# Kernel optimization log

Measured on AMD Instinct MI355X. Metric: run time of the kernel, lower is better.

## Reference

```python
import jax, jax.numpy as jnp
import numpy as np

V, D, E, N, Dd, Dc, NL, B, L = 50280, 1024, 2048, 16, 64, 4, 2, 2, 1024
EPS = 1e-5


def rmsnorm(x, w):
    return x * jax.lax.rsqrt(jnp.mean(x * x, axis=-1, keepdims=True) + EPS) * w


def setup_inputs() -> dict:
    key = jax.random.key(0)
    ks = jax.random.split(key, 18)
    n = jax.random.normal
    inp = {
        "input_ids": jax.random.randint(ks[0], (B, L), 0, V),
        "embedding": n(ks[1], (V, D), jnp.float32) * 0.02,
        "lm_head_w": n(ks[2], (V, D), jnp.float32) * 0.02,
        "norm_w": jnp.ones((D,), jnp.float32),
        # stacked per-layer params (leading dim = n_layer)
        "l_norm_w": jnp.ones((NL, D), jnp.float32),
        "l_skip_w": n(ks[3], (NL, E, D), jnp.float32) / np.sqrt(D),
        "l_in_w": n(ks[4], (NL, E, D), jnp.float32) / np.sqrt(D),
        "l_conv_w": n(ks[5], (NL, E, 1, Dc), jnp.float32) / np.sqrt(Dc),
        "l_conv_b": jnp.zeros((NL, E), jnp.float32),
        "l_Wd1": n(ks[6], (NL, Dd, E), jnp.float32) / np.sqrt(E),
        "l_Wd2_w": n(ks[7], (NL, E, Dd), jnp.float32) / np.sqrt(Dd),
        "l_Wd2_b": n(ks[8], (NL, E), jnp.float32) * 0.1 - 4.0,  # small dt init
        "l_WB": n(ks[9], (NL, N, E), jnp.float32) / np.sqrt(E),
        "l_WC": n(ks[10], (NL, N, E), jnp.float32) / np.sqrt(E),
        "l_A_log": jnp.log(jax.random.uniform(ks[11], (NL, E, N), jnp.float32, 0.5, 1.2)),
        "l_WD": jnp.ones((NL, E), jnp.float32),
        "l_out_w": n(ks[12], (NL, D, E), jnp.float32) / np.sqrt(E),
    }
    return inp


def mamba_layer(resid, norm_w, skip_w, in_w, conv_w, conv_b, Wd1, Wd2_w, Wd2_b,
                WB, WC, A_log, WD, out_w):
    x = rmsnorm(resid, norm_w)                      # [B,L,D]
    skip = x @ skip_w.T                             # [B,L,E]
    x = x @ in_w.T                                  # [B,L,E]
    # depthwise causal conv (pad D_conv-1 on left == pad both + slice [:L])
    xc = jax.lax.conv_general_dilated(
        x.transpose(0, 2, 1), conv_w, (1,), [(Dc - 1, 0)],
        feature_group_count=E, dimension_numbers=("NCH", "OIH", "NCH"))
    x = (xc + conv_b[None, :, None]).transpose(0, 2, 1)  # [B,L,E]
    x = jax.nn.silu(x)

    delta = jax.nn.softplus((x @ Wd1.T) @ Wd2_w.T + Wd2_b)  # [B,L,E]
    A = -jnp.exp(A_log)                                      # [E,N]
    A_bar = jnp.exp(delta[..., None] * A)                    # [B,L,E,N]
    Bt = x @ WB.T                                            # [B,L,N]
    Ct = x @ WC.T                                            # [B,L,N]
    Bx = (delta * x)[..., None] * Bt[:, :, None, :]          # [B,L,E,N]

    def step(h, inp):
        Ab_t, Bx_t, C_t = inp                                # [B,E,N],[B,E,N],[B,N]
        h = Ab_t * h + Bx_t
        y = jnp.einsum("ben,bn->be", h, C_t)
        return h, y

    h0 = jnp.zeros((B, E, N), x.dtype)
    _, ys = jax.lax.scan(step, h0,
                         (A_bar.transpose(1, 0, 2, 3), Bx.transpose(1, 0, 2, 3),
                          Ct.transpose(1, 0, 2)))
    y = ys.transpose(1, 0, 2)                                # [B,L,E]
    y = y + x * WD
    y = y * jax.nn.silu(skip)
    return resid + y @ out_w.T


def reference(input_ids, embedding, lm_head_w, norm_w, l_norm_w, l_skip_w, l_in_w,
              l_conv_w, l_conv_b, l_Wd1, l_Wd2_w, l_Wd2_b, l_WB, l_WC, l_A_log,
              l_WD, l_out_w):
    resid = embedding[input_ids]                             # [B,L,D]
    for i in range(NL):
        resid = mamba_layer(resid, l_norm_w[i], l_skip_w[i], l_in_w[i],
                            l_conv_w[i], l_conv_b[i], l_Wd1[i], l_Wd2_w[i],
                            l_Wd2_b[i], l_WB[i], l_WC[i], l_A_log[i], l_WD[i],
                            l_out_w[i])
    resid = rmsnorm(resid, norm_w)
    return resid @ lm_head_w.T                               # [B,L,V]
```

## Files before the change

kernel.cpp:

```cpp
#include <hip/hip_runtime.h>

typedef unsigned short u16;
using bf16x8 = __attribute__((ext_vector_type(8))) __bf16;
using f32x4  = __attribute__((ext_vector_type(4))) float;

typedef const void __attribute__((address_space(1))) gvoid_t;
typedef void __attribute__((address_space(3))) lvoid_t;

#define NL 2
#define Bd 2
#define Ld 1024
#define Dd_ 1024
#define Ed 2048
#define Nd 16
#define TOK (Bd*Ld)
#define VPAD 50432
#define VREAL 50280
#define NCHUNK 16
#define CLEN 64
#define XLD 4096

__device__ __forceinline__ u16 f2bf(float f) {
    union { float f; unsigned u; } v; v.f = f;
    unsigned u = v.u;
    unsigned r = (u + 0x7fffu + ((u >> 16) & 1u)) >> 16;
    return (u16)r;
}
__device__ __forceinline__ float siluf(float x) { return x / (1.f + __expf(-x)); }
__device__ __forceinline__ float softplusf(float z) {
    return (z > 15.f) ? z : log1pf(__expf(z));
}

__global__ void k_f32_to_bf16(const float* __restrict__ s, u16* __restrict__ d, int n4) {
    int i = blockIdx.x * 256 + threadIdx.x;
    if (i >= n4) return;
    float4 v = *(const float4*)&s[(size_t)i * 4];
    ushort4 o; o.x = f2bf(v.x); o.y = f2bf(v.y); o.z = f2bf(v.z); o.w = f2bf(v.w);
    *(ushort4*)&d[(size_t)i * 4] = o;
}

__global__ void k_f32_to_bf16_pad(const float* __restrict__ s, u16* __restrict__ d,
                                  int n4valid, int n4tot) {
    int i = blockIdx.x * 256 + threadIdx.x;
    if (i >= n4tot) return;
    ushort4 o;
    if (i < n4valid) {
        float4 v = *(const float4*)&s[(size_t)i * 4];
        o.x = f2bf(v.x); o.y = f2bf(v.y); o.z = f2bf(v.z); o.w = f2bf(v.w);
    } else { o.x = o.y = o.z = o.w = 0; }
    *(ushort4*)&d[(size_t)i * 4] = o;
}

__global__ void k_build_wsmall(const float* __restrict__ Wd1, const float* __restrict__ WB,
                               const float* __restrict__ WC, u16* __restrict__ dst) {
    int i = blockIdx.x * 256 + threadIdx.x;
    int col = (i * 4) & (Ed - 1);
    int r = (i * 4) >> 11;
    ushort4 o;
    const float* src = nullptr;
    if (r < 64) src = &Wd1[(size_t)r * Ed];
    else if (r < 80) src = &WB[(size_t)(r - 64) * Ed];
    else if (r < 96) src = &WC[(size_t)(r - 80) * Ed];
    if (src) {
        float4 v = *(const float4*)&src[col];
        o.x = f2bf(v.x); o.y = f2bf(v.y); o.z = f2bf(v.z); o.w = f2bf(v.w);
    } else { o.x = o.y = o.z = o.w = 0; }
    *(ushort4*)&dst[(size_t)i * 4] = o;
}

__global__ void k_embed(const int* __restrict__ ids, const float* __restrict__ emb,
                        float* __restrict__ resid) {
    int tk = blockIdx.x;
    int d = threadIdx.x * 4;
    int id = ids[tk];
    float4 v = *(const float4*)&emb[(size_t)id * Dd_ + d];
    *(float4*)&resid[(size_t)tk * Dd_ + d] = v;
}

__global__ void k_rmsnorm_bf16(const float* __restrict__ in, const float* __restrict__ w,
                               u16* __restrict__ out) {
    int tk = blockIdx.x;
    int tid = threadIdx.x;
    float4 v = *(const float4*)&in[(size_t)tk * Dd_ + tid * 4];
    float ss = v.x * v.x + v.y * v.y + v.z * v.z + v.w * v.w;
    #pragma unroll
    for (int m = 32; m; m >>= 1) ss += __shfl_xor(ss, m);
    __shared__ float red[4];
    if ((tid & 63) == 0) red[tid >> 6] = ss;
    __syncthreads();
    ss = red[0] + red[1] + red[2] + red[3];
    float rs = rsqrtf(ss * (1.f / 1024.f) + 1e-5f);
    float4 wv = *(const float4*)&w[tid * 4];
    ushort4 o;
    o.x = f2bf(v.x * rs * wv.x); o.y = f2bf(v.y * rs * wv.y);
    o.z = f2bf(v.z * rs * wv.z); o.w = f2bf(v.w * rs * wv.w);
    *(ushort4*)&out[(size_t)tk * Dd_ + tid * 4] = o;
}

__global__ void k_conv_silu(const float* __restrict__ xin, const float* __restrict__ cw,
                            const float* __restrict__ cb, float* __restrict__ xout,
                            u16* __restrict__ xbf) {
    int blk = blockIdx.x;
    int tk = blk >> 1;
    int e0 = ((blk & 1) << 10) + threadIdx.x * 4;
    int b = tk >> 10, l = tk & 1023;
    float4 w0 = *(const float4*)&cw[(size_t)(e0 + 0) * 4];
    float4 w1 = *(const float4*)&cw[(size_t)(e0 + 1) * 4];
    float4 w2 = *(const float4*)&cw[(size_t)(e0 + 2) * 4];
    float4 w3 = *(const float4*)&cw[(size_t)(e0 + 3) * 4];
    float4 bv = *(const float4*)&cb[e0];
    float a0 = bv.x, a1 = bv.y, a2 = bv.z, a3 = bv.w;
    const float* wp0 = (const float*)&w0; const float* wp1 = (const float*)&w1;
    const float* wp2 = (const float*)&w2; const float* wp3 = (const float*)&w3;
    #pragma unroll
    for (int k = 0; k < 4; ++k) {
        int ll = l - 3 + k;
        if (ll < 0) continue;
        float4 xv = *(const float4*)&xin[((size_t)(b * 1024 + ll)) * XLD + e0];
        a0 = fmaf(xv.x, wp0[k], a0); a1 = fmaf(xv.y, wp1[k], a1);
        a2 = fmaf(xv.z, wp2[k], a2); a3 = fmaf(xv.w, wp3[k], a3);
    }
    a0 = siluf(a0); a1 = siluf(a1); a2 = siluf(a2); a3 = siluf(a3);
    float4 o; o.x = a0; o.y = a1; o.z = a2; o.w = a3;
    *(float4*)&xout[(size_t)tk * Ed + e0] = o;
    ushort4 ob; ob.x = f2bf(a0); ob.y = f2bf(a1); ob.z = f2bf(a2); ob.w = f2bf(a3);
    *(ushort4*)&xbf[(size_t)tk * Ed + e0] = ob;
}

__global__ void k_reduce_xs(const float* __restrict__ part, float* __restrict__ xs,
                            u16* __restrict__ xsbf) {
    size_t i4 = ((size_t)blockIdx.x * 256 + threadIdx.x) * 4;
    float4 s = *(const float4*)&part[i4];
    #pragma unroll
    for (int c = 1; c < 8; ++c) {
        float4 v = *(const float4*)&part[(size_t)c * TOK * 128 + i4];
        s.x += v.x; s.y += v.y; s.z += v.z; s.w += v.w;
    }
    *(float4*)&xs[i4] = s;
    ushort4 o; o.x = f2bf(s.x); o.y = f2bf(s.y); o.z = f2bf(s.z); o.w = f2bf(s.w);
    *(ushort4*)&xsbf[i4] = o;
}

__global__ void k_add2(const float* __restrict__ part, float* __restrict__ resid) {
    size_t i4 = ((size_t)blockIdx.x * 256 + threadIdx.x) * 4;
    float4 r = *(const float4*)&resid[i4];
    float4 a = *(const float4*)&part[i4];
    float4 b = *(const float4*)&part[(size_t)TOK * Dd_ + i4];
    r.x += a.x + b.x; r.y += a.y + b.y; r.z += a.z + b.z; r.w += a.w + b.w;
    *(float4*)&resid[i4] = r;
}

__global__ void k_scan_pass1(const float* __restrict__ delta, const float* __restrict__ x,
                             const float* __restrict__ xs, const float* __restrict__ A_log,
                             float* __restrict__ sumd, float* __restrict__ Hc) {
    __shared__ float sBt[CLEN][16];
    int t = blockIdx.x * 256 + threadIdx.x;
    int e = t & (Ed - 1);
    int cb = t >> 11;
    int b = cb & 1, c = cb >> 1;
    int rowbase = b * 1024 + c * CLEN;
    {
        int f = threadIdx.x * 4;
        int row = f >> 4, cc = f & 15;
        float4 v = *(const float4*)&xs[(size_t)(rowbase + row) * 128 + 64 + cc];
        *(float4*)&sBt[row][cc] = v;
    }
    __syncthreads();
    float dA[16], h[16];
    #pragma unroll
    for (int n = 0; n < 16; ++n) { dA[n] = -__expf(A_log[e * 16 + n]); h[n] = 0.f; }
    float sd = 0.f;
    for (int l = 0; l < CLEN; ++l) {
        size_t row = (size_t)rowbase + l;
        float dlt = delta[row * Ed + e];
        float xv  = x[row * Ed + e];
        sd += dlt;
        float dx = dlt * xv;
        float4 bt0 = *(const float4*)&sBt[l][0];
        float4 bt1 = *(const float4*)&sBt[l][4];
        float4 bt2 = *(const float4*)&sBt[l][8];
        float4 bt3 = *(const float4*)&sBt[l][12];
        float bts[16] = {bt0.x,bt0.y,bt0.z,bt0.w, bt1.x,bt1.y,bt1.z,bt1.w,
                         bt2.x,bt2.y,bt2.z,bt2.w, bt3.x,bt3.y,bt3.z,bt3.w};
        #pragma unroll
        for (int n = 0; n < 16; ++n) {
            float a = __expf(dA[n] * dlt);
            h[n] = fmaf(a, h[n], dx * bts[n]);
        }
    }
    size_t gg = (size_t)cb * Ed + e;
    #pragma unroll
    for (int n = 0; n < 16; ++n) Hc[gg * 16 + n] = h[n];
    sumd[gg] = sd;
}

__global__ void k_scan_combine(const float* __restrict__ sumd, const float* __restrict__ Hc,
                               const float* __restrict__ A_log, float* __restrict__ Hin) {
    int idx = blockIdx.x * 256 + threadIdx.x;
    int n = idx & 15;
    int e = (idx >> 4) & (Ed - 1);
    int b = idx >> 15;
    float dA = -__expf(A_log[e * Nd + n]);
    float h = 0.f;
    #pragma unroll
    for (int c = 0; c < NCHUNK; ++c) {
        size_t g = ((size_t)(c * Bd + b) * Ed + e);
        Hin[g * Nd + n] = h;
        float a = __expf(dA * sumd[g]);
        h = fmaf(a, h, Hc[g * Nd + n]);
    }
}

__global__ void k_scan_pass2(const float* __restrict__ delta, const float* __restrict__ x,
                             const float* __restrict__ xs, const float* __restrict__ A_log,
                             const float* __restrict__ Hin, const float* __restrict__ WD,
                             const float* __restrict__ skipg, u16* __restrict__ ybf) {
    __shared__ float sBC[CLEN][32];
    int t = blockIdx.x * 256 + threadIdx.x;
    int e = t & (Ed - 1);
    int cb = t >> 11;
    int b = cb & 1, c = cb >> 1;
    int rowbase = b * 1024 + c * CLEN;
    {
        int f = threadIdx.x * 8;
        int row = f >> 5, cc = f & 31;
        float4 v0 = *(const float4*)&xs[(size_t)(rowbase + row) * 128 + 64 + cc];
        float4 v1 = *(const float4*)&xs[(size_t)(rowbase + row) * 128 + 64 + cc + 4];
        *(float4*)&sBC[row][cc] = v0;
        *(float4*)&sBC[row][cc + 4] = v1;
    }
    __syncthreads();
    float dA[16], h[16];
    size_t gg = (size_t)cb * Ed + e;
    #pragma unroll
    for (int n = 0; n < 16; ++n) {
        dA[n] = -__expf(A_log[e * 16 + n]);
        h[n] = Hin[gg * 16 + n];
    }
    float wd = WD[e];
    for (int l = 0; l < CLEN; ++l) {
        size_t row = (size_t)rowbase + l;
        float dlt = delta[row * Ed + e];
        float xv  = x[row * Ed + e];
        float dx = dlt * xv;
        float4 b0 = *(const float4*)&sBC[l][0];
        float4 b1 = *(const float4*)&sBC[l][4];
        float4 b2 = *(const float4*)&sBC[l][8];
        float4 b3 = *(const float4*)&sBC[l][12];
        float4 c0 = *(const float4*)&sBC[l][16];
        float4 c1 = *(const float4*)&sBC[l][20];
        float4 c2 = *(const float4*)&sBC[l][24];
        float4 c3 = *(const float4*)&sBC[l][28];
        float bts[16] = {b0.x,b0.y,b0.z,b0.w, b1.x,b1.y,b1.z,b1.w,
                         b2.x,b2.y,b2.z,b2.w, b3.x,b3.y,b3.z,b3.w};
        float cts[16] = {c0.x,c0.y,c0.z,c0.w, c1.x,c1.y,c1.z,c1.w,
                         c2.x,c2.y,c2.z,c2.w, c3.x,c3.y,c3.z,c3.w};
        float y = 0.f;
        #pragma unroll
        for (int n = 0; n < 16; ++n) {
            float a = __expf(dA[n] * dlt);
            h[n] = fmaf(a, h[n], dx * bts[n]);
            y = fmaf(h[n], cts[n], y);
        }
        float yo = y + xv * wd;
        float sk = skipg[row * XLD + e];
        ybf[row * Ed + e] = f2bf(yo * siluf(sk));
    }
}

template<int EPI>
__global__ __launch_bounds__(256, 2)
void k_gemm_bt(const u16* __restrict__ A, int lda,
               const u16* __restrict__ B, int ldb,
               float* __restrict__ C, int ldc,
               const float* __restrict__ aux,
               int ntm, int Nstore, int Kc, size_t Cz) {
    __shared__ u16 lsA[2][128 * 32];
    __shared__ u16 lsB[2][128 * 32];
    int kz = blockIdx.z;
    A += (size_t)kz * Kc;
    B += (size_t)kz * Kc;
    C += (size_t)kz * Cz;
    int tid = threadIdx.x;
    int bid = blockIdx.x;
    int mt = bid % ntm, nt = bid / ntm;
    int mBase = mt * 128, nBase = nt * 128;
    int lane = tid & 63, wid = tid >> 6;
    int wr = wid >> 1, wc = wid & 1;

    f32x4 acc[4][4] = {};
    const u16* Ablk = A + (size_t)mBase * lda;
    const u16* Bblk = B + (size_t)nBase * ldb;
    int nk = Kc >> 5;

    auto stage = [&](int buf, int kt) {
        #pragma unroll
        for (int i = 0; i < 2; ++i) {
            int chunk = i * 256 + tid;
            int row = chunk >> 2;
            int kc  = (chunk & 3) << 3;
            const u16* ga = Ablk + (size_t)row * lda + (kt << 5) + kc;
            const u16* gb = Bblk + (size_t)row * ldb + (kt << 5) + kc;
            u16* la = &lsA[buf][(size_t)(i * 256 + wid * 64) * 8];
            u16* lb = &lsB[buf][(size_t)(i * 256 + wid * 64) * 8];
            __builtin_amdgcn_global_load_lds((gvoid_t*)ga, (lvoid_t*)la, 16, 0, 0);
            __builtin_amdgcn_global_load_lds((gvoid_t*)gb, (lvoid_t*)lb, 16, 0, 0);
        }
    };
    auto compute = [&](int buf) {
        bf16x8 af[4], bfr[4];
        const u16* baseA = lsA[buf];
        const u16* baseB = lsB[buf];
        int kq = (lane >> 4) << 3;
        int r  = lane & 15;
        #pragma unroll
        for (int mi = 0; mi < 4; ++mi)
            af[mi] = *(const bf16x8*)&baseA[(size_t)((wr * 64 + mi * 16 + r) * 32 + kq)];
        #pragma unroll
        for (int ni = 0; ni < 4; ++ni)
            bfr[ni] = *(const bf16x8*)&baseB[(size_t)((wc * 64 + ni * 16 + r) * 32 + kq)];
        #pragma unroll
        for (int mi = 0; mi < 4; ++mi)
            #pragma unroll
            for (int ni = 0; ni < 4; ++ni)
                acc[mi][ni] = __builtin_amdgcn_mfma_f32_16x16x32_bf16(af[mi], bfr[ni], acc[mi][ni], 0, 0, 0);
    };

    stage(0, 0);
    asm volatile("s_waitcnt vmcnt(0)" ::: "memory");
    __syncthreads();
    int cur = 0;
    for (int kt = 0; kt + 1 < nk; ++kt) {
        stage(cur ^ 1, kt + 1);
        compute(cur);
        asm volatile("s_waitcnt vmcnt(0)" ::: "memory");
        __syncthreads();
        cur ^= 1;
    }
    compute(cur);

    int rbase = (lane >> 4) * 4, ccol = lane & 15;
    #pragma unroll
    for (int mi = 0; mi < 4; ++mi) {
        #pragma unroll
        for (int ni = 0; ni < 4; ++ni) {
            int gc = nBase + wc * 64 + ni * 16 + ccol;
            if (gc < Nstore) {
                float bias = (EPI == 2) ? aux[gc] : 0.f;
                #pragma unroll
                for (int rr = 0; rr < 4; ++rr) {
                    int gr = mBase + wr * 64 + mi * 16 + rbase + rr;
                    size_t off = (size_t)gr * ldc + gc;
                    float v = acc[mi][ni][rr];
                    if (EPI == 2) v = softplusf(v + bias);
                    C[off] = v;
                }
            }
        }
    }
}

#define BAR()    asm volatile("s_barrier" ::: "memory")
#define WAITV2() asm volatile("s_waitcnt vmcnt(2)" ::: "memory")
#define WAITV0() asm volatile("s_waitcnt vmcnt(0)" ::: "memory")

#define STG(buf, mat, h, kt) { \
    const u16* _s0 = ((mat) ? srcB[(h)*2]     : srcA[(h)*2])     + (size_t)(kt) * 64; \
    const u16* _s1 = ((mat) ? srcB[(h)*2 + 1] : srcA[(h)*2 + 1]) + (size_t)(kt) * 64; \
    char* _d = (char*)&ls[buf][mat][0]; \
    __builtin_amdgcn_global_load_lds((gvoid_t*)_s0, (lvoid_t*)(_d + (h)*16384 + tid*16), 16, 0, 0); \
    __builtin_amdgcn_global_load_lds((gvoid_t*)_s1, (lvoid_t*)(_d + (h)*16384 + 8192 + tid*16), 16, 0, 0); }

#define QUAD(buf, kk, mih) { \
    const char* _pa = (const char*)&ls[buf][0][0]; \
    const char* _pb = (const char*)&ls[buf][1][0]; \
    bf16x8 _af[4], _bf[4]; \
    _Pragma("unroll") \
    for (int _m = 0; _m < 4; ++_m) \
        _af[_m] = *(const bf16x8*)(_pa + abase + ((mih)*4 + _m) * 2048 + (kk) * 1024); \
    _Pragma("unroll") \
    for (int _n = 0; _n < 4; ++_n) \
        _bf[_n] = *(const bf16x8*)(_pb + bbase + _n * 2048 + (kk) * 1024); \
    __builtin_amdgcn_s_setprio(1); \
    _Pragma("unroll") \
    for (int _m = 0; _m < 4; ++_m) \
        _Pragma("unroll") \
        for (int _n = 0; _n < 4; ++_n) \
            acc[(mih)*4 + _m][_n] = __builtin_amdgcn_mfma_f32_16x16x32_bf16(_af[_m], _bf[_n], acc[(mih)*4 + _m][_n], 0, 0, 0); \
    __builtin_amdgcn_s_setprio(0); }

__global__ __launch_bounds__(512, 2)
void k_gemm256(const u16* __restrict__ A, int lda,
               const u16* __restrict__ B, int ldb,
               float* __restrict__ C, int ldc,
               int ntm, int Nstore, int K) {
    __shared__ u16 ls[2][2][256 * 64];
    const int tid = threadIdx.x;
    const int lane = tid & 63, wid = tid >> 6;
    const int wr = wid >> 2, wc = wid & 3;

    int nwg = gridDim.x, bid = blockIdx.x;
    int q8 = nwg >> 3, r8 = nwg & 7;
    int xcd = bid & 7, linb = bid >> 3;
    int sb = (xcd < r8 ? xcd * (q8 + 1) : r8 * (q8 + 1) + (xcd - r8) * q8) + linb;
    int mt = sb % ntm, nt = sb / ntm;

    const u16* Ablk = A + (size_t)(mt * 256) * lda;
    const u16* Bblk = B + (size_t)(nt * 256) * ldb;

    const u16* srcA[4]; const u16* srcB[4];
    #pragma unroll
    for (int s = 0; s < 4; ++s) {
        int p = s * 8192 + tid * 16;
        int qq = p ^ (((p >> 9) & 1) << 5);
        int sub = qq >> 10, rin = (qq >> 6) & 15, cby = qq & 63;
        int row = ((sub >> 1) << 4) | rin;
        int col = ((((sub & 1) << 6) | cby)) >> 1;
        srcA[s] = Ablk + (size_t)row * lda + col;
        srcB[s] = Bblk + (size_t)row * ldb + col;
    }
    int l15 = lane & 15;
    int lowb = (l15 * 64 + ((lane >> 4) << 4)) ^ (((l15 >> 3) & 1) << 5);
    int abase = wr * 16384 + lowb;
    int bbase = wc * 8192  + lowb;

    f32x4 acc[8][4] = {};
    int nk = K >> 6, nit = nk >> 1;

    STG(0, 0, 0, 0); STG(0, 0, 1, 0); STG(0, 1, 0, 0); STG(0, 1, 1, 0);

    for (int i = 0; i < nit; ++i) {
        int t1 = 2 * i + 1, t2 = 2 * i + 2;
        bool more = (i + 1 < nit);
        STG(1, 0, 0, t1);
        WAITV2(); BAR();
        QUAD(0, 0, 0); BAR();
        STG(1, 0, 1, t1);
        QUAD(0, 0, 1); BAR();
        STG(1, 1, 0, t1);
        QUAD(0, 1, 0); BAR();
        STG(1, 1, 1, t1);
        QUAD(0, 1, 1); BAR();
        if (more) { STG(0, 0, 0, t2); WAITV2(); } else { WAITV0(); }
        BAR();
        QUAD(1, 0, 0); BAR();
        if (more) STG(0, 0, 1, t2);
        QUAD(1, 0, 1); BAR();
        if (more) STG(0, 1, 0, t2);
        QUAD(1, 1, 0); BAR();
        if (more) STG(0, 1, 1, t2);
        QUAD(1, 1, 1); BAR();
    }

    int rb = (lane >> 4) * 4, cc = lane & 15;
    int mrow = mt * 256 + wr * 128, ncol = nt * 256 + wc * 64;
    #pragma unroll
    for (int mi = 0; mi < 8; ++mi) {
        #pragma unroll
        for (int ni = 0; ni < 4; ++ni) {
            int gc = ncol + ni * 16 + cc;
            if (gc < Nstore) {
                #pragma unroll
                for (int rr = 0; rr < 4; ++rr) {
                    size_t off = (size_t)(mrow + mi * 16 + rb + rr) * ldc + gc;
                    C[off] = acc[mi][ni][rr];
                }
            }
        }
    }
}

extern "C" void kernel_launch(void* const* d_in, const int* in_sizes, int n_in,
                              void* d_out, int out_size, void* d_ws, size_t ws_size,
                              hipStream_t stream) {
    const int*   ids   = (const int*)d_in[0];
    const float* emb   = (const float*)d_in[1];
    const float* lmw   = (const float*)d_in[2];
    const float* normw = (const float*)d_in[3];
    const float* lnw   = (const float*)d_in[4];
    const float* lskip = (const float*)d_in[5];
    const float* linw  = (const float*)d_in[6];
    const float* lcw   = (const float*)d_in[7];
    const float* lcb   = (const float*)d_in[8];
    const float* lWd1  = (const float*)d_in[9];
    const float* lWd2  = (const float*)d_in[10];
    const float* lWd2b = (const float*)d_in[11];
    const float* lWB   = (const float*)d_in[12];
    const float* lWC   = (const float*)d_in[13];
    const float* lAlog = (const float*)d_in[14];
    const float* lWD   = (const float*)d_in[15];
    const float* loutw = (const float*)d_in[16];
    float* out = (float*)d_out;

    char* ws = (char*)d_ws;
    size_t off = 0;
    auto alloc = [&](size_t bytes) { char* p = ws + off; off += (bytes + 255) & ~(size_t)255; return p; };
    u16*   lm_bf    = (u16*)  alloc((size_t)VPAD * 1024 * 2);
    u16*   wsi_bf   = (u16*)  alloc((size_t)NL * 4096 * Dd_ * 2);
    u16*   wout_bf  = (u16*)  alloc((size_t)NL * Dd_ * Ed * 2);
    u16*   wd2_bf   = (u16*)  alloc((size_t)NL * Ed * 64 * 2);
    u16*   wsml_bf  = (u16*)  alloc((size_t)NL * 128 * Ed * 2);
    float* resid    = (float*)alloc((size_t)TOK * Dd_ * 4);
    u16*   xn_bf    = (u16*)  alloc((size_t)TOK * Dd_ * 2);
    float* xall     = (float*)alloc((size_t)TOK * XLD * 4);
    float* xf       = (float*)alloc((size_t)TOK * Ed * 4);
    u16*   xbf      = (u16*)  alloc((size_t)TOK * Ed * 2);
    float* xs       = (float*)alloc((size_t)TOK * 128 * 4);
    u16*   xs_bf    = (u16*)  alloc((size_t)TOK * 128 * 2);
    float* xs_part  = (float*)alloc((size_t)8 * TOK * 128 * 4);
    float* opart    = (float*)alloc((size_t)2 * TOK * Dd_ * 4);
    float* delta    = (float*)alloc((size_t)TOK * Ed * 4);
    float* sumd     = (float*)alloc((size_t)NCHUNK * Bd * Ed * 4);
    float* Hc       = (float*)alloc((size_t)NCHUNK * Bd * Ed * Nd * 4);
    float* Hin      = (float*)alloc((size_t)NCHUNK * Bd * Ed * Nd * 4);
    u16*   ybf      = (u16*)  alloc((size_t)TOK * Ed * 2);
    (void)ws_size; (void)in_sizes; (void)n_in; (void)out_size;

    {
        int n4v = VREAL * 1024 / 4, n4t = VPAD * 1024 / 4;
        k_f32_to_bf16_pad<<<(n4t + 255) / 256, 256, 0, stream>>>(lmw, lm_bf, n4v, n4t);
        int n4 = Ed * Dd_ / 4;
        for (int lyr = 0; lyr < NL; ++lyr) {
            k_f32_to_bf16<<<(n4 + 255) / 256, 256, 0, stream>>>(
                lskip + (size_t)lyr * Ed * Dd_, wsi_bf + (size_t)lyr * 4096 * Dd_, n4);
            k_f32_to_bf16<<<(n4 + 255) / 256, 256, 0, stream>>>(
                linw + (size_t)lyr * Ed * Dd_, wsi_bf + (size_t)lyr * 4096 * Dd_ + (size_t)Ed * Dd_, n4);
        }
        k_f32_to_bf16<<<(NL * n4 + 255) / 256, 256, 0, stream>>>(loutw, wout_bf, NL * n4);
        int n4b = NL * Ed * 64 / 4;
        k_f32_to_bf16<<<(n4b + 255) / 256, 256, 0, stream>>>(lWd2, wd2_bf, n4b);
        for (int lyr = 0; lyr < NL; ++lyr)
            k_build_wsmall<<<256, 256, 0, stream>>>(lWd1 + (size_t)lyr * 64 * Ed,
                                                    lWB + (size_t)lyr * Nd * Ed,
                                                    lWC + (size_t)lyr * Nd * Ed,
                                                    wsml_bf + (size_t)lyr * 128 * Ed);
    }

    k_embed<<<TOK, 256, 0, stream>>>(ids, emb, resid);

    for (int lyr = 0; lyr < NL; ++lyr) {
        const float* Alog = lAlog + (size_t)lyr * Ed * Nd;
        k_rmsnorm_bf16<<<TOK, 256, 0, stream>>>(resid, lnw + (size_t)lyr * Dd_, xn_bf);
        k_gemm_bt<0><<<dim3(16 * 32, 1, 1), 256, 0, stream>>>(xn_bf, Dd_,
            wsi_bf + (size_t)lyr * 4096 * Dd_, Dd_, xall, XLD, nullptr, 16, 4096, 1024, 0);
        k_conv_silu<<<TOK * 2, 256, 0, stream>>>(xall + Ed, lcw + (size_t)lyr * Ed * 4,
                                                 lcb + (size_t)lyr * Ed, xf, xbf);
        k_gemm_bt<0><<<dim3(16, 1, 8), 256, 0, stream>>>(xbf, Ed,
            wsml_bf + (size_t)lyr * 128 * Ed, Ed, xs_part, 128, nullptr, 16, 128, 256,
            (size_t)TOK * 128);
        k_reduce_xs<<<TOK * 128 / 4 / 256, 256, 0, stream>>>(xs_part, xs, xs_bf);
        k_gemm_bt<2><<<dim3(16 * 16, 1, 1), 256, 0, stream>>>(xs_bf, 128,
            wd2_bf + (size_t)lyr * Ed * 64, 64, delta, Ed, lWd2b + (size_t)lyr * Ed,
            16, Ed, 64, 0);
        k_scan_pass1<<<NCHUNK * Bd * Ed / 256, 256, 0, stream>>>(delta, xf, xs, Alog, sumd, Hc);
        k_scan_combine<<<Bd * Ed * Nd / 256, 256, 0, stream>>>(sumd, Hc, Alog, Hin);
        k_scan_pass2<<<NCHUNK * Bd * Ed / 256, 256, 0, stream>>>(delta, xf, xs, Alog, Hin,
            lWD + (size_t)lyr * Ed, xall, ybf);
        k_gemm_bt<0><<<dim3(16 * 8, 1, 2), 256, 0, stream>>>(ybf, Ed,
            wout_bf + (size_t)lyr * Dd_ * Ed, Ed, opart, Dd_, nullptr, 16, Dd_, 1024,
            (size_t)TOK * Dd_);
        k_add2<<<TOK * Dd_ / 4 / 256, 256, 0, stream>>>(opart, resid);
    }

    k_rmsnorm_bf16<<<TOK, 256, 0, stream>>>(resid, normw, xn_bf);
    k_gemm256<<<dim3(8 * (VPAD / 256), 1, 1), 512, 0, stream>>>(xn_bf, Dd_, lm_bf, Dd_,
        out, VREAL, 8, VREAL, 1024);
}
```

Baseline: 811.7 us.

## Fuse weight conversions, embed+norm, add+norm, and fold scan combine into pass2

All weight fp32-to-bf16 conversions are merged into a single launch, and the embedding gather is fused with the first RMSNorm. The residual add is fused with the next layer's (or the final) RMSNorm. The separate chunk-state combine kernel is removed: each pass2 thread recomputes its incoming state by looping over the earlier chunks. This cuts launch count and intermediate traffic, at the cost of redundant serial prefix work in pass2 for later chunks.

```diff
diff --git a/kernel.cpp b/kernel.cpp
--- a/kernel.cpp
+++ b/kernel.cpp
@@ -31,57 +31,60 @@
     return (z > 15.f) ? z : log1pf(__expf(z));
 }
 
-__global__ void k_f32_to_bf16(const float* __restrict__ s, u16* __restrict__ d, int n4) {
-    int i = blockIdx.x * 256 + threadIdx.x;
-    if (i >= n4) return;
-    float4 v = *(const float4*)&s[(size_t)i * 4];
-    ushort4 o; o.x = f2bf(v.x); o.y = f2bf(v.y); o.z = f2bf(v.z); o.w = f2bf(v.w);
-    *(ushort4*)&d[(size_t)i * 4] = o;
-}
-
-__global__ void k_f32_to_bf16_pad(const float* __restrict__ s, u16* __restrict__ d,
-                                  int n4valid, int n4tot) {
-    int i = blockIdx.x * 256 + threadIdx.x;
-    if (i >= n4tot) return;
+__global__ void k_convert_all(const float* __restrict__ lmw, const float* __restrict__ lskip,
+                              const float* __restrict__ linw, const float* __restrict__ loutw,
+                              const float* __restrict__ lWd2, const float* __restrict__ lWd1,
+                              const float* __restrict__ lWB, const float* __restrict__ lWC,
+                              u16* __restrict__ lm_bf, u16* __restrict__ wsi_bf,
+                              u16* __restrict__ wout_bf, u16* __restrict__ wd2_bf,
+                              u16* __restrict__ wsml_bf) {
+    int g = blockIdx.x * 256 + threadIdx.x;
+    const float* src = nullptr; u16* dst = nullptr;
+    if (g < 12910592) {
+        dst = lm_bf + (size_t)g * 4;
+        if (g < 12871680) src = lmw + (size_t)g * 4;
+    } else if (g < 15007744) {
+        int i = g - 12910592;
+        int layer = i >> 20;
+        int within = i & 1048575;
+        int mat = within >> 19;
+        int idx = within & 524287;
+        src = (mat ? linw : lskip) + ((size_t)layer << 21) + ((size_t)idx * 4);
+        dst = wsi_bf + ((size_t)layer << 22) + ((size_t)mat << 21) + ((size_t)idx * 4);
+    } else if (g < 16056320) {
+        int i = g - 15007744;
+        src = loutw + (size_t)i * 4; dst = wout_bf + (size_t)i * 4;
+    } else if (g < 16121856) {
+        int i = g - 16056320;
+        src = lWd2 + (size_t)i * 4; dst = wd2_bf + (size_t)i * 4;
+    } else {
+        int i = g - 16121856;
+        int layer = i >> 16;
+        int j = i & 65535;
+        int col = (j * 4) & 2047;
+        int r = (j * 4) >> 11;
+        const float* s2 = nullptr;
+        if (r < 64) s2 = lWd1 + ((size_t)layer * 64 + r) * 2048;
+        else if (r < 80) s2 = lWB + ((size_t)layer * 16 + (r - 64)) * 2048;
+        else if (r < 96) s2 = lWC + ((size_t)layer * 16 + (r - 80)) * 2048;
+        dst = wsml_bf + ((size_t)layer << 18) + (size_t)j * 4;
+        if (s2) src = s2 + col;
+    }
     ushort4 o;
-    if (i < n4valid) {
-        float4 v = *(const float4*)&s[(size_t)i * 4];
+    if (src) {
+        float4 v = *(const float4*)src;
         o.x = f2bf(v.x); o.y = f2bf(v.y); o.z = f2bf(v.z); o.w = f2bf(v.w);
     } else { o.x = o.y = o.z = o.w = 0; }
-    *(ushort4*)&d[(size_t)i * 4] = o;
-}
-
-__global__ void k_build_wsmall(const float* __restrict__ Wd1, const float* __restrict__ WB,
-                               const float* __restrict__ WC, u16* __restrict__ dst) {
-    int i = blockIdx.x * 256 + threadIdx.x;
-    int col = (i * 4) & (Ed - 1);
-    int r = (i * 4) >> 11;
-    ushort4 o;
-    const float* src = nullptr;
-    if (r < 64) src = &Wd1[(size_t)r * Ed];
-    else if (r < 80) src = &WB[(size_t)(r - 64) * Ed];
-    else if (r < 96) src = &WC[(size_t)(r - 80) * Ed];
-    if (src) {
-        float4 v = *(const float4*)&src[col];
-        o.x = f2bf(v.x); o.y = f2bf(v.y); o.z = f2bf(v.z); o.w = f2bf(v.w);
-    } else { o.x = o.y = o.z = o.w = 0; }
-    *(ushort4*)&dst[(size_t)i * 4] = o;
-}
-
-__global__ void k_embed(const int* __restrict__ ids, const float* __restrict__ emb,
-                        float* __restrict__ resid) {
-    int tk = blockIdx.x;
-    int d = threadIdx.x * 4;
+    *(ushort4*)dst = o;
+}
+
+__global__ void k_embed_norm(const int* __restrict__ ids, const float* __restrict__ emb,
+                             const float* __restrict__ w, float* __restrict__ resid,
+                             u16* __restrict__ out) {
+    int tk = blockIdx.x, tid = threadIdx.x;
     int id = ids[tk];
-    float4 v = *(const float4*)&emb[(size_t)id * Dd_ + d];
-    *(float4*)&resid[(size_t)tk * Dd_ + d] = v;
-}
-
-__global__ void k_rmsnorm_bf16(const float* __restrict__ in, const float* __restrict__ w,
-                               u16* __restrict__ out) {
-    int tk = blockIdx.x;
-    int tid = threadIdx.x;
-    float4 v = *(const float4*)&in[(size_t)tk * Dd_ + tid * 4];
+    float4 v = *(const float4*)&emb[(size_t)id * Dd_ + tid * 4];
+    *(float4*)&resid[(size_t)tk * Dd_ + tid * 4] = v;
     float ss = v.x * v.x + v.y * v.y + v.z * v.z + v.w * v.w;
     #pragma unroll
     for (int m = 32; m; m >>= 1) ss += __shfl_xor(ss, m);
@@ -94,6 +97,30 @@
     ushort4 o;
     o.x = f2bf(v.x * rs * wv.x); o.y = f2bf(v.y * rs * wv.y);
     o.z = f2bf(v.z * rs * wv.z); o.w = f2bf(v.w * rs * wv.w);
+    *(ushort4*)&out[(size_t)tk * Dd_ + tid * 4] = o;
+}
+
+__global__ void k_add2_norm(const float* __restrict__ part, float* __restrict__ resid,
+                            const float* __restrict__ w, u16* __restrict__ out) {
+    int tk = blockIdx.x, tid = threadIdx.x;
+    size_t i4 = (size_t)tk * Dd_ + tid * 4;
+    float4 r = *(const float4*)&resid[i4];
+    float4 a = *(const float4*)&part[i4];
+    float4 b = *(const float4*)&part[(size_t)TOK * Dd_ + i4];
+    r.x += a.x + b.x; r.y += a.y + b.y; r.z += a.z + b.z; r.w += a.w + b.w;
+    *(float4*)&resid[i4] = r;
+    float ss = r.x * r.x + r.y * r.y + r.z * r.z + r.w * r.w;
+    #pragma unroll
+    for (int m = 32; m; m >>= 1) ss += __shfl_xor(ss, m);
+    __shared__ float red[4];
+    if ((tid & 63) == 0) red[tid >> 6] = ss;
+    __syncthreads();
+    ss = red[0] + red[1] + red[2] + red[3];
+    float rs = rsqrtf(ss * (1.f / 1024.f) + 1e-5f);
+    float4 wv = *(const float4*)&w[tid * 4];
+    ushort4 o;
+    o.x = f2bf(r.x * rs * wv.x); o.y = f2bf(r.y * rs * wv.y);
+    o.z = f2bf(r.z * rs * wv.z); o.w = f2bf(r.w * rs * wv.w);
     *(ushort4*)&out[(size_t)tk * Dd_ + tid * 4] = o;
 }
 
@@ -141,15 +168,6 @@
     *(ushort4*)&xsbf[i4] = o;
 }
 
-__global__ void k_add2(const float* __restrict__ part, float* __restrict__ resid) {
-    size_t i4 = ((size_t)blockIdx.x * 256 + threadIdx.x) * 4;
-    float4 r = *(const float4*)&resid[i4];
-    float4 a = *(const float4*)&part[i4];
-    float4 b = *(const float4*)&part[(size_t)TOK * Dd_ + i4];
-    r.x += a.x + b.x; r.y += a.y + b.y; r.z += a.z + b.z; r.w += a.w + b.w;
-    *(float4*)&resid[i4] = r;
-}
-
 __global__ void k_scan_pass1(const float* __restrict__ delta, const float* __restrict__ x,
                              const float* __restrict__ xs, const float* __restrict__ A_log,
                              float* __restrict__ sumd, float* __restrict__ Hc) {
@@ -194,26 +212,10 @@
     sumd[gg] = sd;
 }
 
-__global__ void k_scan_combine(const float* __restrict__ sumd, const float* __restrict__ Hc,
-                               const float* __restrict__ A_log, float* __restrict__ Hin) {
-    int idx = blockIdx.x * 256 + threadIdx.x;
-    int n = idx & 15;
-    int e = (idx >> 4) & (Ed - 1);
-    int b = idx >> 15;
-    float dA = -__expf(A_log[e * Nd + n]);
-    float h = 0.f;
-    #pragma unroll
-    for (int c = 0; c < NCHUNK; ++c) {
-        size_t g = ((size_t)(c * Bd + b) * Ed + e);
-        Hin[g * Nd + n] = h;
-        float a = __expf(dA * sumd[g]);
-        h = fmaf(a, h, Hc[g * Nd + n]);
-    }
-}
-
 __global__ void k_scan_pass2(const float* __restrict__ delta, const float* __restrict__ x,
                              const float* __restrict__ xs, const float* __restrict__ A_log,
-                             const float* __restrict__ Hin, const float* __restrict__ WD,
+                             const float* __restrict__ sumd, const float* __restrict__ Hc,
+                             const float* __restrict__ WD,
                              const float* __restrict__ skipg, u16* __restrict__ ybf) {
     __shared__ float sBC[CLEN][32];
     int t = blockIdx.x * 256 + threadIdx.x;
@@ -231,11 +233,17 @@
     }
     __syncthreads();
     float dA[16], h[16];
-    size_t gg = (size_t)cb * Ed + e;
     #pragma unroll
     for (int n = 0; n < 16; ++n) {
         dA[n] = -__expf(A_log[e * 16 + n]);
-        h[n] = Hin[gg * 16 + n];
+        h[n] = 0.f;
+    }
+    for (int cc = 0; cc < c; ++cc) {
+        size_t g2 = ((size_t)(cc * Bd + b) * Ed + e);
+        float sdc = sumd[g2];
+        #pragma unroll
+        for (int n = 0; n < 16; ++n)
+            h[n] = fmaf(__expf(dA[n] * sdc), h[n], Hc[g2 * 16 + n]);
     }
     float wd = WD[e];
     for (int l = 0; l < CLEN; ++l) {
@@ -512,35 +520,16 @@
     float* delta    = (float*)alloc((size_t)TOK * Ed * 4);
     float* sumd     = (float*)alloc((size_t)NCHUNK * Bd * Ed * 4);
     float* Hc       = (float*)alloc((size_t)NCHUNK * Bd * Ed * Nd * 4);
-    float* Hin      = (float*)alloc((size_t)NCHUNK * Bd * Ed * Nd * 4);
     u16*   ybf      = (u16*)  alloc((size_t)TOK * Ed * 2);
     (void)ws_size; (void)in_sizes; (void)n_in; (void)out_size;
 
-    {
-        int n4v = VREAL * 1024 / 4, n4t = VPAD * 1024 / 4;
-        k_f32_to_bf16_pad<<<(n4t + 255) / 256, 256, 0, stream>>>(lmw, lm_bf, n4v, n4t);
-        int n4 = Ed * Dd_ / 4;
-        for (int lyr = 0; lyr < NL; ++lyr) {
-            k_f32_to_bf16<<<(n4 + 255) / 256, 256, 0, stream>>>(
-                lskip + (size_t)lyr * Ed * Dd_, wsi_bf + (size_t)lyr * 4096 * Dd_, n4);
-            k_f32_to_bf16<<<(n4 + 255) / 256, 256, 0, stream>>>(
-                linw + (size_t)lyr * Ed * Dd_, wsi_bf + (size_t)lyr * 4096 * Dd_ + (size_t)Ed * Dd_, n4);
-        }
-        k_f32_to_bf16<<<(NL * n4 + 255) / 256, 256, 0, stream>>>(loutw, wout_bf, NL * n4);
-        int n4b = NL * Ed * 64 / 4;
-        k_f32_to_bf16<<<(n4b + 255) / 256, 256, 0, stream>>>(lWd2, wd2_bf, n4b);
-        for (int lyr = 0; lyr < NL; ++lyr)
-            k_build_wsmall<<<256, 256, 0, stream>>>(lWd1 + (size_t)lyr * 64 * Ed,
-                                                    lWB + (size_t)lyr * Nd * Ed,
-                                                    lWC + (size_t)lyr * Nd * Ed,
-                                                    wsml_bf + (size_t)lyr * 128 * Ed);
-    }
-
-    k_embed<<<TOK, 256, 0, stream>>>(ids, emb, resid);
+    k_convert_all<<<63488, 256, 0, stream>>>(lmw, lskip, linw, loutw, lWd2, lWd1, lWB, lWC,
+                                             lm_bf, wsi_bf, wout_bf, wd2_bf, wsml_bf);
+
+    k_embed_norm<<<TOK, 256, 0, stream>>>(ids, emb, lnw, resid, xn_bf);
 
     for (int lyr = 0; lyr < NL; ++lyr) {
         const float* Alog = lAlog + (size_t)lyr * Ed * Nd;
-        k_rmsnorm_bf16<<<TOK, 256, 0, stream>>>(resid, lnw + (size_t)lyr * Dd_, xn_bf);
         k_gemm_bt<0><<<dim3(16 * 32, 1, 1), 256, 0, stream>>>(xn_bf, Dd_,
             wsi_bf + (size_t)lyr * 4096 * Dd_, Dd_, xall, XLD, nullptr, 16, 4096, 1024, 0);
         k_conv_silu<<<TOK * 2, 256, 0, stream>>>(xall + Ed, lcw + (size_t)lyr * Ed * 4,
@@ -553,16 +542,15 @@
             wd2_bf + (size_t)lyr * Ed * 64, 64, delta, Ed, lWd2b + (size_t)lyr * Ed,
             16, Ed, 64, 0);
         k_scan_pass1<<<NCHUNK * Bd * Ed / 256, 256, 0, stream>>>(delta, xf, xs, Alog, sumd, Hc);
-        k_scan_combine<<<Bd * Ed * Nd / 256, 256, 0, stream>>>(sumd, Hc, Alog, Hin);
-        k_scan_pass2<<<NCHUNK * Bd * Ed / 256, 256, 0, stream>>>(delta, xf, xs, Alog, Hin,
-            lWD + (size_t)lyr * Ed, xall, ybf);
+        k_scan_pass2<<<NCHUNK * Bd * Ed / 256, 256, 0, stream>>>(delta, xf, xs, Alog,
+            sumd, Hc, lWD + (size_t)lyr * Ed, xall, ybf);
         k_gemm_bt<0><<<dim3(16 * 8, 1, 2), 256, 0, stream>>>(ybf, Ed,
             wout_bf + (size_t)lyr * Dd_ * Ed, Ed, opart, Dd_, nullptr, 16, Dd_, 1024,
             (size_t)TOK * Dd_);
-        k_add2<<<TOK * Dd_ / 4 / 256, 256, 0, stream>>>(opart, resid);
-    }
-
-    k_rmsnorm_bf16<<<TOK, 256, 0, stream>>>(resid, normw, xn_bf);
+        const float* nw = (lyr == NL - 1) ? normw : lnw + (size_t)(lyr + 1) * Dd_;
+        k_add2_norm<<<TOK, 256, 0, stream>>>(opart, resid, nw, xn_bf);
+    }
+
     k_gemm256<<<dim3(8 * (VPAD / 256), 1, 1), 512, 0, stream>>>(xn_bf, Dd_, lm_bf, Dd_,
         out, VREAL, 8, VREAL, 1024);
 }
```

Measured after the change: 802.8 us. About the same (-1.1%).
